# Performance work log

Measured on AMD Instinct MI355X. Metric: run time of the kernel, lower is better.

The kernel has to match this reference:

```python
import jax, jax.numpy as jnp
import numpy as np

N_FM = 100000; N_TP = 4096; N_SM = 100000
IN_FM = 64; IN_SM = 32; IN_TP = 32; IN_GF = 64; HID = 128
E_QOQ = 1000000; E_BP = 1000000; E_CP = 500000; E_CD = 500000; E_RB = 1000000


def setup_inputs():
    key = jax.random.key(0)
    ks = jax.random.split(key, 32)
    rn = lambda k, s, sc=0.05: jax.random.normal(k, s, jnp.float32) * sc
    inp = {}
    inp['x_fm'] = jax.random.normal(ks[0], (N_FM, IN_FM), jnp.float32)
    inp['x_sm'] = jax.random.normal(ks[1], (N_SM, IN_SM), jnp.float32)
    inp['period_vol'] = jax.random.uniform(ks[2], (N_TP, 1), jnp.float32)
    inp['gf'] = jax.random.normal(ks[3], (1, IN_GF), jnp.float32)
    inp['pe_table'] = rn(ks[4], (N_TP, IN_TP), 1.0)  # period_emb weight
    inp['qoq_src'] = jax.random.randint(ks[5], (E_QOQ,), 0, N_FM)
    inp['qoq_dst'] = jax.random.randint(ks[6], (E_QOQ,), 0, N_FM)
    inp['bp_src'] = jax.random.randint(ks[7], (E_BP,), 0, N_FM)
    inp['bp_dst'] = jax.random.randint(ks[8], (E_BP,), 0, N_TP)
    inp['cp_src'] = jax.random.randint(ks[9], (E_CP,), 0, N_TP)
    inp['cp_dst'] = jax.random.randint(ks[10], (E_CP,), 0, N_FM)
    inp['cd_src'] = jax.random.randint(ks[11], (E_CD,), 0, N_TP)
    inp['cd_dst'] = jax.random.randint(ks[12], (E_CD,), 0, N_SM)
    inp['rb_src'] = jax.random.randint(ks[13], (E_RB,), 0, N_TP)
    inp['rb_dst'] = jax.random.randint(ks[14], (E_RB,), 0, N_FM)
    i = 15
    # per-relation SAGEConv params: W_l [in_src,H] + bias, W_r [in_dst,H] (root, no bias)
    for name, ins, ind in [('qoq', IN_FM, IN_FM), ('bp', IN_FM, IN_TP), ('cp', IN_TP, IN_FM), ('cd', IN_TP, IN_SM), ('rb', IN_TP, IN_FM)]:
        inp[name + '_Wl'] = rn(ks[i], (ins, HID)); inp[name + '_bl'] = jnp.zeros((HID,), jnp.float32)
        inp[name + '_Wr'] = rn(ks[i + 1], (ind, HID)); i += 2
    for t in ['fm', 'tp', 'sm']:
        inp['ln_' + t + '_g'] = jnp.ones((HID,), jnp.float32)
        inp['ln_' + t + '_b'] = jnp.zeros((HID,), jnp.float32)
    inp['head_W1'] = rn(ks[i], (HID * 3 + IN_GF, HID // 2)); inp['head_b1'] = jnp.zeros((HID // 2,), jnp.float32)
    inp['head_W2'] = rn(ks[i + 1], (HID // 2, 1)); inp['head_b2'] = jnp.zeros((1,), jnp.float32)
    return inp


def _seg_mean(feat, dst, n):
    s = jax.ops.segment_sum(feat, dst, num_segments=n)
    c = jax.ops.segment_sum(jnp.ones((dst.shape[0], 1), feat.dtype), dst, num_segments=n)
    return s / jnp.maximum(c, 1.0)


def _sage(x_src, x_dst, src, dst, Wl, bl, Wr):
    # PyG SAGEConv: lin_l(mean_j x_j) + lin_r(x_i); aggregate raw features, then transform
    m = _seg_mean(x_src[src], dst, x_dst.shape[0])
    return m @ Wl + bl + x_dst @ Wr


def _ln(x, g, b, eps=1e-5):
    mu = x.mean(-1, keepdims=True)
    xc = x - mu
    var = (xc * xc).mean(-1, keepdims=True)
    return xc / jnp.sqrt(var + eps) * g + b


def _forward(x_fm, x_sm, period_vol, gf, pe_table,
             qoq_Wl, qoq_bl, qoq_Wr, bp_Wl, bp_bl, bp_Wr, cp_Wl, cp_bl, cp_Wr,
             cd_Wl, cd_bl, cd_Wr, rb_Wl, rb_bl, rb_Wr,
             ln_fm_g, ln_fm_b, ln_tp_g, ln_tp_b, ln_sm_g, ln_sm_b,
             head_W1, head_b1, head_W2, head_b2,
             qoq_src, qoq_dst, bp_src, bp_dst, cp_src, cp_dst, cd_src, cd_dst, rb_src, rb_dst):
    pe = pe_table * period_vol  # [T, in_tp]
    # HeteroConv aggr='mean': average relation outputs per destination type
    out_fm = (_sage(x_fm, x_fm, qoq_src, qoq_dst, qoq_Wl, qoq_bl, qoq_Wr)
              + _sage(pe, x_fm, cp_src, cp_dst, cp_Wl, cp_bl, cp_Wr)
              + _sage(pe, x_fm, rb_src, rb_dst, rb_Wl, rb_bl, rb_Wr)) / 3.0
    out_tp = _sage(x_fm, pe, bp_src, bp_dst, bp_Wl, bp_bl, bp_Wr)
    out_sm = _sage(pe, x_sm, cd_src, cd_dst, cd_Wl, cd_bl, cd_Wr)
    fm = jax.nn.relu(_ln(out_fm, ln_fm_g, ln_fm_b))
    tp = jax.nn.relu(_ln(out_tp, ln_tp_g, ln_tp_b))
    sm = jax.nn.relu(_ln(out_sm, ln_sm_g, ln_sm_b))
    h = jnp.concatenate([fm.mean(0), tp.mean(0), sm.mean(0), gf[0]], axis=-1)
    h = jax.nn.relu(h @ head_W1 + head_b1)  # dropout is identity in eval
    return (h @ head_W2 + head_b2).squeeze()


def reference(x_fm, x_sm, period_vol, gf, pe_table,
              qoq_src, qoq_dst, bp_src, bp_dst, cp_src, cp_dst, cd_src, cd_dst, rb_src, rb_dst,
              qoq_Wl, qoq_bl, qoq_Wr, bp_Wl, bp_bl, bp_Wr, cp_Wl, cp_bl, cp_Wr,
              cd_Wl, cd_bl, cd_Wr, rb_Wl, rb_bl, rb_Wr,
              ln_fm_g, ln_fm_b, ln_tp_g, ln_tp_b, ln_sm_g, ln_sm_b,
              head_W1, head_b1, head_W2, head_b2):
    return _forward(x_fm, x_sm, period_vol, gf, pe_table,
                    qoq_Wl, qoq_bl, qoq_Wr, bp_Wl, bp_bl, bp_Wr, cp_Wl, cp_bl, cp_Wr,
                    cd_Wl, cd_bl, cd_Wr, rb_Wl, rb_bl, rb_Wr,
                    ln_fm_g, ln_fm_b, ln_tp_g, ln_tp_b, ln_sm_g, ln_sm_b,
                    head_W1, head_b1, head_W2, head_b2,
                    qoq_src, qoq_dst, bp_src, bp_dst, cp_src, cp_dst, cd_src, cd_dst, rb_src, rb_dst)
```

## Files before the change

kernel.cpp:

```cpp
#include <hip/hip_runtime.h>
#include <hip/hip_fp16.h>

#define N_FM 100000
#define N_TP 4096
#define N_SM 100000
#define HID 128
#define E_QOQ 1000000
#define E_BP 1000000
#define E_CP 500000
#define E_CD 500000
#define E_RB 1000000
#define E_TOT 4000000

#define EO_CP  1000000
#define EO_RB  1500000
#define EO_BP  2500000
#define EO_CD  3500000

#define EL_QOQ 0
#define EL_CP  (N_FM)
#define EL_RB  (2 * N_FM)
#define EL_BP  (3 * N_FM)
#define EL_CD  (3 * N_FM + N_TP)
#define NTOT   (3 * N_FM + N_TP + N_SM)

#define BB_QOQ 0
#define BB_CP  782
#define BB_RB  1173
#define BB_BP  1564
#define BB_CD  1692
#define NBUCK  2083
#define CHUNK  4096
#define NCHUNK ((E_TOT + CHUNK - 1) / CHUNK)
#define EPB    (CHUNK / 256)

#define PAIRS_CAP 5784064

#define GRID_FM 768
#define GRID_TP 64
#define GRID_SM 1024

__device__ __forceinline__ int bucket_base(int b) {
    if (b < BB_CP) return b * 2048;
    if (b < BB_RB) return 1601536 + (b - BB_CP) * 2048;
    if (b < BB_BP) return 2402304 + (b - BB_RB) * 3584;
    if (b < BB_CD) return 3803648 + (b - BB_BP) * 9216;
    return 4983296 + (b - BB_CD) * 2048;
}

typedef _Float16 h2 __attribute__((ext_vector_type(2)));
typedef _Float16 f16x8_t __attribute__((ext_vector_type(8)));
typedef float f32x4_t __attribute__((ext_vector_type(4)));

union U32H2 { unsigned u; h2 h; };
union U4H8 { uint4 u; f16x8_t h; };

#if defined(__has_builtin)
#if __has_builtin(__builtin_amdgcn_fdot2)
#define HAVE_FDOT2 1
#endif
#endif

__device__ __forceinline__ unsigned pk2(float a, float b) {
    U32H2 x; x.h = h2{(_Float16)a, (_Float16)b}; return x.u;
}
__device__ __forceinline__ f16x8_t as_h8(uint4 v) { U4H8 x; x.u = v; return x.h; }

__device__ __forceinline__ float dot2sel(float acc, h2 v, h2 sel) {
#ifdef HAVE_FDOT2
    return __builtin_amdgcn_fdot2(v, sel, acc, false);
#else
    return acc + (float)v[0] * (float)sel[0] + (float)v[1] * (float)sel[1];
#endif
}

#define R1 (N_FM * 16)
#define R2 (R1 + N_SM * 8)
#define R3 (R2 + N_TP * 8)
#define R4 (R3 + 12288)
#define R5 (R4 + 6144)
#define R6 (R5 + 4096)
#define R7 (R6 + 128)

__device__ __forceinline__ unsigned pack_pair(const float* W, int p, int c) {
    return pk2(W[(2 * p) * HID + c], W[(2 * p + 1) * HID + c]);
}

__global__ void pack_all(const float* __restrict__ x_fm, const float* __restrict__ x_sm,
                         const float* __restrict__ pe_table, const float* __restrict__ pvol,
                         const float* __restrict__ qoq_Wl, const float* __restrict__ cp_Wl,
                         const float* __restrict__ rb_Wl, const float* __restrict__ qoq_Wr,
                         const float* __restrict__ cp_Wr, const float* __restrict__ rb_Wr,
                         const float* __restrict__ bp_Wl, const float* __restrict__ bp_Wr,
                         const float* __restrict__ cd_Wl, const float* __restrict__ cd_Wr,
                         const float* __restrict__ qoq_bl, const float* __restrict__ cp_bl,
                         const float* __restrict__ rb_bl,
                         unsigned* __restrict__ x_fm_f, unsigned* __restrict__ x_sm_f,
                         unsigned* __restrict__ pe_f, unsigned* __restrict__ wf_fm,
                         unsigned* __restrict__ wf_tp, unsigned* __restrict__ wf_sm,
                         float* __restrict__ bias_fm) {
    int gid = blockIdx.x * blockDim.x + threadIdx.x;
    if (gid < R1) {
        float4 t = ((const float4*)x_fm)[gid];
        uint2 o; o.x = pk2(t.x, t.y); o.y = pk2(t.z, t.w);
        ((uint2*)x_fm_f)[gid] = o;
    } else if (gid < R2) {
        int i = gid - R1;
        float4 t = ((const float4*)x_sm)[i];
        uint2 o; o.x = pk2(t.x, t.y); o.y = pk2(t.z, t.w);
        ((uint2*)x_sm_f)[i] = o;
    } else if (gid < R3) {
        int i = gid - R2;
        float4 t = ((const float4*)pe_table)[i];
        float v = pvol[i >> 3];
        uint2 o; o.x = pk2(t.x * v, t.y * v); o.y = pk2(t.z * v, t.w * v);
        ((uint2*)pe_f)[i] = o;
    } else if (gid < R4) {
        int j = gid - R3;
        int f = j >> 8, lr = (j >> 2) & 63, jj = j & 3;
        int p = (f >> 3) * 16 + ((lr >> 4) << 2) + jj;
        int c = (f & 7) * 16 + (lr & 15);
        unsigned v;
        if (p < 32) v = pack_pair(qoq_Wl, p, c);
        else if (p < 48) v = pack_pair(cp_Wl, p - 32, c);
        else if (p < 64) v = pack_pair(rb_Wl, p - 48, c);
        else {
            int pp = p - 64;
            float u0 = qoq_Wr[(2 * pp) * HID + c] + cp_Wr[(2 * pp) * HID + c] + rb_Wr[(2 * pp) * HID + c];
            float u1 = qoq_Wr[(2 * pp + 1) * HID + c] + cp_Wr[(2 * pp + 1) * HID + c] + rb_Wr[(2 * pp + 1) * HID + c];
            v = pk2(u0, u1);
        }
        wf_fm[j] = v;
    } else if (gid < R5) {
        int j = gid - R4;
        int f = j >> 8, lr = (j >> 2) & 63, jj = j & 3;
        int p = (f >> 3) * 16 + ((lr >> 4) << 2) + jj;
        int c = (f & 7) * 16 + (lr & 15);
        wf_tp[j] = (p < 32) ? pack_pair(bp_Wl, p, c) : pack_pair(bp_Wr, p - 32, c);
    } else if (gid < R6) {
        int j = gid - R5;
        int f = j >> 8, lr = (j >> 2) & 63, jj = j & 3;
        int p = (f >> 3) * 16 + ((lr >> 4) << 2) + jj;
        int c = (f & 7) * 16 + (lr & 15);
        wf_sm[j] = (p < 16) ? pack_pair(cd_Wl, p, c) : pack_pair(cd_Wr, p - 16, c);
    } else if (gid < R7) {
        int c = gid - R6;
        bias_fm[c] = qoq_bl[c] + cp_bl[c] + rb_bl[c];
    }
}

struct EdgePtrs {
    const int *qs, *qd, *cs, *cd_, *rs, *rd, *bs, *bd, *ds, *dd;
};

template <bool NEED_SRC>
__device__ __forceinline__ void edge_decode(const EdgePtrs& P, int e, int& bucket, int& dl, int& src) {
    const int* dp = P.qd; const int* sp = P.qs;
    int i = e, bb = BB_QOQ, sh = 7;
    if (e >= EO_CP) { i = e - EO_CP; dp = P.cd_; sp = P.cs; bb = BB_CP; sh = 8; }
    if (e >= EO_RB) { i = e - EO_RB; dp = P.rd;  sp = P.rs; bb = BB_RB; sh = 8; }
    if (e >= EO_BP) { i = e - EO_BP; dp = P.bd;  sp = P.bs; bb = BB_BP; sh = 5; }
    if (e >= EO_CD) { i = e - EO_CD; dp = P.dd;  sp = P.ds; bb = BB_CD; sh = 8; }
    int d = dp[i];
    bucket = bb + (d >> sh);
    dl = d & ((1 << sh) - 1);
    if (NEED_SRC) src = sp[i];
}

__global__ void __launch_bounds__(256) bin_kernel(EdgePtrs P, int* __restrict__ bwork,
                                                  unsigned* __restrict__ pairs) {
    __shared__ int lh[NBUCK];
    const int tid = threadIdx.x;
    for (int i = tid; i < NBUCK; i += 256) lh[i] = 0;
    __syncthreads();
    const int base = blockIdx.x * CHUNK;
    const int lim = min(base + CHUNK, E_TOT);
    unsigned ebd[EPB]; int esr[EPB];
#pragma unroll
    for (int j = 0; j < EPB; j++) {
        int e = base + tid + j * 256;
        if (e < lim) {
            int b, dl, s;
            edge_decode<true>(P, e, b, dl, s);
            ebd[j] = ((unsigned)b << 8) | (unsigned)dl;
            esr[j] = s;
            atomicAdd(&lh[b], 1);
        }
    }
    __syncthreads();
#pragma unroll
    for (int u = 0; u < (NBUCK + 255) / 256; u++) {
        int b = tid + u * 256;
        if (b < NBUCK) {
            int c = lh[b];
            lh[b] = c ? bucket_base(b) + atomicAdd(&bwork[b], c) : 0;
        }
    }
    __syncthreads();
#pragma unroll
    for (int j = 0; j < EPB; j++) {
        int e = base + tid + j * 256;
        if (e < lim) {
            int b = (int)(ebd[j] >> 8);
            int pos = atomicAdd(&lh[b], 1);
            pairs[pos] = ((ebd[j] & 255u) << 24) | (unsigned)esr[j];
        }
    }
}

__global__ void __launch_bounds__(256) esort(const int* __restrict__ bwork,
                                             const unsigned* __restrict__ pairs,
                                             int* __restrict__ so,
                                             int* __restrict__ el_beg, int* __restrict__ el_end) {
    __shared__ int hist[256];
    __shared__ int wsum[4];
    __shared__ int so_lds[9216];
    const int b = blockIdx.x;
    const int tid = threadIdx.x;
    const int lane = tid & 63, wv = tid >> 6;
    int beg = bucket_base(b);
    int end = beg + bwork[b];
    int egbase, ne;
    if (b < BB_CP)      { int e0 = (b - BB_QOQ) << 7; egbase = EL_QOQ + e0; ne = min(128, N_FM - e0); }
    else if (b < BB_RB) { int e0 = (b - BB_CP) << 8;  egbase = EL_CP + e0;  ne = min(256, N_FM - e0); }
    else if (b < BB_BP) { int e0 = (b - BB_RB) << 8;  egbase = EL_RB + e0;  ne = min(256, N_FM - e0); }
    else if (b < BB_CD) { int e0 = (b - BB_BP) << 5;  egbase = EL_BP + e0;  ne = min(32, N_TP - e0); }
    else                { int e0 = (b - BB_CD) << 8;  egbase = EL_CD + e0;  ne = min(256, N_SM - e0); }
    hist[tid] = 0;
    __syncthreads();
    for (int e = beg + tid; e < end; e += 256)
        atomicAdd(&hist[pairs[e] >> 24], 1);
    __syncthreads();
    int v = hist[tid];
    int x = v;
#pragma unroll
    for (int off = 1; off < 64; off <<= 1) {
        int u = __shfl_up(x, off);
        if (lane >= off) x += u;
    }
    if (lane == 63) wsum[wv] = x;
    __syncthreads();
    int wbase = 0;
#pragma unroll
    for (int w = 0; w < 4; w++) wbase += (w < wv) ? wsum[w] : 0;
    int excl = wbase + x - v;
    if (tid < ne) {
        el_beg[egbase + tid] = beg + excl;
        el_end[egbase + tid] = beg + excl + v;
    }
    hist[tid] = excl;
    __syncthreads();
    for (int e = beg + tid; e < end; e += 256) {
        unsigned pr = pairs[e];
        int dl = pr >> 24;
        int pos = atomicAdd(&hist[dl], 1);
        so_lds[pos] = (int)(pr & 0xFFFFFF);
    }
    __syncthreads();
    const int n = end - beg;
    for (int i = tid; i < n; i += 256) so[beg + i] = so_lds[i];
}

template <int LOGP, int NPRO>
__device__ __forceinline__ void gather_one(int g, int lane, const int* __restrict__ begs,
                                           const int* __restrict__ ends,
                                           const int* __restrict__ ssrc,
                                           const unsigned* __restrict__ feat,
                                           unsigned* __restrict__ mean) {
    const int P = 1 << LOGP;
    const h2 SLO = h2{(_Float16)1.0f, (_Float16)0.0f};
    const h2 SHI = h2{(_Float16)0.0f, (_Float16)1.0f};
    int beg = begs[g], end = ends[g];
    int n = end - beg;
    float alo = 0.0f, ahi = 0.0f;
    if (n > 0) {
        const int nm1 = n - 1;
        int s[NPRO];
#pragma unroll
        for (int j = 0; j < NPRO; j++) s[j] = ssrc[beg + min(j, nm1)];
        unsigned v[NPRO];
#pragma unroll
        for (int j = 0; j < NPRO; j++) v[j] = feat[(size_t)(unsigned)s[j] * P + lane];
#pragma unroll
        for (int j = 0; j < NPRO; j++) {
            U32H2 u; u.u = (j < n) ? v[j] : 0u;
            alo = dot2sel(alo, u.h, SLO); ahi = dot2sel(ahi, u.h, SHI);
        }
        int i = beg + NPRO;
        for (; i + 8 <= end; i += 8) {
            int t0 = ssrc[i],     t1 = ssrc[i + 1], t2 = ssrc[i + 2], t3 = ssrc[i + 3];
            int t4 = ssrc[i + 4], t5 = ssrc[i + 5], t6 = ssrc[i + 6], t7 = ssrc[i + 7];
            unsigned w0 = feat[(size_t)t0 * P + lane];
            unsigned w1 = feat[(size_t)t1 * P + lane];
            unsigned w2 = feat[(size_t)t2 * P + lane];
            unsigned w3 = feat[(size_t)t3 * P + lane];
            unsigned w4 = feat[(size_t)t4 * P + lane];
            unsigned w5 = feat[(size_t)t5 * P + lane];
            unsigned w6 = feat[(size_t)t6 * P + lane];
            unsigned w7 = feat[(size_t)t7 * P + lane];
            U32H2 u;
            u.u = w0; alo = dot2sel(alo, u.h, SLO); ahi = dot2sel(ahi, u.h, SHI);
            u.u = w1; alo = dot2sel(alo, u.h, SLO); ahi = dot2sel(ahi, u.h, SHI);
            u.u = w2; alo = dot2sel(alo, u.h, SLO); ahi = dot2sel(ahi, u.h, SHI);
            u.u = w3; alo = dot2sel(alo, u.h, SLO); ahi = dot2sel(ahi, u.h, SHI);
            u.u = w4; alo = dot2sel(alo, u.h, SLO); ahi = dot2sel(ahi, u.h, SHI);
            u.u = w5; alo = dot2sel(alo, u.h, SLO); ahi = dot2sel(ahi, u.h, SHI);
            u.u = w6; alo = dot2sel(alo, u.h, SLO); ahi = dot2sel(ahi, u.h, SHI);
            u.u = w7; alo = dot2sel(alo, u.h, SLO); ahi = dot2sel(ahi, u.h, SHI);
        }
        for (; i < end; i++) {
            U32H2 u; u.u = feat[(size_t)ssrc[i] * P + lane];
            alo = dot2sel(alo, u.h, SLO); ahi = dot2sel(ahi, u.h, SHI);
        }
    }
    float ic = (n > 0) ? 1.0f / (float)n : 0.0f;
    mean[(size_t)g * P + lane] = pk2(alo * ic, ahi * ic);
}

#define G1 (N_TP * 32)
#define G2 (G1 + N_FM * 32)
#define G3 (G2 + N_FM * 16)
#define G4 (G3 + N_SM * 16)
#define G5 (G4 + N_FM * 16)

__global__ void __launch_bounds__(256)
gather_all(const int* __restrict__ el_beg, const int* __restrict__ el_end,
           const int* __restrict__ so_all,
           const unsigned* __restrict__ x_fm_f, const unsigned* __restrict__ pe_f,
           unsigned* __restrict__ mean_qoq, unsigned* __restrict__ mean_cp,
           unsigned* __restrict__ mean_rb, unsigned* __restrict__ mean_bp,
           unsigned* __restrict__ mean_cd) {
    int gid = blockIdx.x * blockDim.x + threadIdx.x;
    if (gid < G1) {
        gather_one<5, 16>(gid >> 5, gid & 31, el_beg + EL_BP, el_end + EL_BP, so_all, x_fm_f, mean_bp);
    } else if (gid < G2) {
        int i = gid - G1;
        gather_one<5, 16>(i >> 5, i & 31, el_beg + EL_QOQ, el_end + EL_QOQ, so_all, x_fm_f, mean_qoq);
    } else if (gid < G3) {
        int i = gid - G2;
        gather_one<4, 8>(i >> 4, i & 15, el_beg + EL_CP, el_end + EL_CP, so_all, pe_f, mean_cp);
    } else if (gid < G4) {
        int i = gid - G3;
        gather_one<4, 8>(i >> 4, i & 15, el_beg + EL_CD, el_end + EL_CD, so_all, pe_f, mean_cd);
    } else if (gid < G5) {
        int i = gid - G4;
        gather_one<4, 16>(i >> 4, i & 15, el_beg + EL_RB, el_end + EL_RB, so_all, pe_f, mean_rb);
    }
}


__global__ void __launch_bounds__(256)
fm_mfma(const unsigned* __restrict__ mq, const unsigned* __restrict__ mc,
        const unsigned* __restrict__ mr, const unsigned* __restrict__ xf,
        const unsigned* __restrict__ wfrag, const float* __restrict__ bias,
        const float* __restrict__ ln_g, const float* __restrict__ ln_b,
        float* __restrict__ part) {
    __shared__ uint4 wlds[48 * 64];
    const int tid = threadIdx.x, lane = tid & 63, wid = tid >> 6;
    for (int i = tid; i < 48 * 64; i += 256) wlds[i] = ((const uint4*)wfrag)[i];
    const int c0 = lane & 15, ko = lane >> 4;
    float bias_[8], g_[8], b_[8], colacc[8];
#pragma unroll
    for (int nt = 0; nt < 8; nt++) {
        int c = nt * 16 + c0;
        bias_[nt] = bias[c]; g_[nt] = ln_g[c]; b_[nt] = ln_b[c]; colacc[nt] = 0.0f;
    }
    __syncthreads();
    const f32x4_t zero = {0.0f, 0.0f, 0.0f, 0.0f};
    const int ntiles = N_FM / 16;
    for (int tile = blockIdx.x * 4 + wid; tile < ntiles; tile += gridDim.x * 4) {
        const size_t row = (size_t)tile * 16 + c0;
        uint4 av[6];
        av[0] = ((const uint4*)mq)[row * 8 + ko];
        av[1] = ((const uint4*)mq)[row * 8 + 4 + ko];
        av[2] = ((const uint4*)mc)[row * 4 + ko];
        av[3] = ((const uint4*)mr)[row * 4 + ko];
        av[4] = ((const uint4*)xf)[row * 8 + ko];
        av[5] = ((const uint4*)xf)[row * 8 + 4 + ko];
        f32x4_t acc[8];
#pragma unroll
        for (int nt = 0; nt < 8; nt++) acc[nt] = zero;
#pragma unroll
        for (int ks = 0; ks < 6; ks++) {
            f16x8_t af = as_h8(av[ks]);
#pragma unroll
            for (int nt = 0; nt < 8; nt++)
                acc[nt] = __builtin_amdgcn_mfma_f32_16x16x32_f16(
                    af, as_h8(wlds[(ks * 8 + nt) * 64 + lane]), acc[nt], 0, 0, 0);
        }
#pragma unroll
        for (int r = 0; r < 4; r++) {
            float yv[8]; float s = 0.0f, q = 0.0f;
#pragma unroll
            for (int nt = 0; nt < 8; nt++) {
                float y = (acc[nt][r] + bias_[nt]) * (1.0f / 3.0f);
                yv[nt] = y; s += y; q += y * y;
            }
#pragma unroll
            for (int off = 1; off < 16; off <<= 1) { s += __shfl_xor(s, off); q += __shfl_xor(q, off); }
            float mu = s * (1.0f / 128.0f);
            float var = fmaxf(q * (1.0f / 128.0f) - mu * mu, 0.0f);
            float rs = rsqrtf(var + 1e-5f);
#pragma unroll
            for (int nt = 0; nt < 8; nt++)
                colacc[nt] += fmaxf((yv[nt] - mu) * rs * g_[nt] + b_[nt], 0.0f);
        }
    }
#pragma unroll
    for (int nt = 0; nt < 8; nt++) {
        colacc[nt] += __shfl_xor(colacc[nt], 16);
        colacc[nt] += __shfl_xor(colacc[nt], 32);
    }
    __syncthreads();
    float* sred = (float*)wlds;
    if (lane < 16) {
#pragma unroll
        for (int nt = 0; nt < 8; nt++) sred[wid * 128 + nt * 16 + lane] = colacc[nt];
    }
    __syncthreads();
    if (tid < 128)
        part[(size_t)blockIdx.x * 128 + tid] =
            sred[tid] + sred[128 + tid] + sred[256 + tid] + sred[384 + tid];
}

template <int KSA, int KSB>
__global__ void __launch_bounds__(256)
rows_mfma(int ntiles, const unsigned* __restrict__ mA, const unsigned* __restrict__ xB,
          const unsigned* __restrict__ wfrag, const float* __restrict__ bl,
          const float* __restrict__ ln_g, const float* __restrict__ ln_b,
          float* __restrict__ part) {
    constexpr int KS = KSA + KSB;
    __shared__ uint4 wlds[KS * 8 * 64];
    const int tid = threadIdx.x, lane = tid & 63, wid = tid >> 6;
    for (int i = tid; i < KS * 8 * 64; i += 256) wlds[i] = ((const uint4*)wfrag)[i];
    const int c0 = lane & 15, ko = lane >> 4;
    float bias_[8], g_[8], b_[8], colacc[8];
#pragma unroll
    for (int nt = 0; nt < 8; nt++) {
        int c = nt * 16 + c0;
        bias_[nt] = bl[c]; g_[nt] = ln_g[c]; b_[nt] = ln_b[c]; colacc[nt] = 0.0f;
    }
    __syncthreads();
    const f32x4_t zero = {0.0f, 0.0f, 0.0f, 0.0f};
    for (int tile = blockIdx.x * 4 + wid; tile < ntiles; tile += gridDim.x * 4) {
        const size_t row = (size_t)tile * 16 + c0;
        uint4 av[KS];
#pragma unroll
        for (int ks = 0; ks < KSA; ks++) av[ks] = ((const uint4*)mA)[row * (KSA * 4) + ks * 4 + ko];
#pragma unroll
        for (int ks = 0; ks < KSB; ks++) av[KSA + ks] = ((const uint4*)xB)[row * (KSB * 4) + ks * 4 + ko];
        f32x4_t acc[8];
#pragma unroll
        for (int nt = 0; nt < 8; nt++) acc[nt] = zero;
#pragma unroll
        for (int ks = 0; ks < KS; ks++) {
            f16x8_t af = as_h8(av[ks]);
#pragma unroll
            for (int nt = 0; nt < 8; nt++)
                acc[nt] = __builtin_amdgcn_mfma_f32_16x16x32_f16(
                    af, as_h8(wlds[(ks * 8 + nt) * 64 + lane]), acc[nt], 0, 0, 0);
        }
#pragma unroll
        for (int r = 0; r < 4; r++) {
            float yv[8]; float s = 0.0f, q = 0.0f;
#pragma unroll
            for (int nt = 0; nt < 8; nt++) {
                float y = acc[nt][r] + bias_[nt];
                yv[nt] = y; s += y; q += y * y;
            }
#pragma unroll
            for (int off = 1; off < 16; off <<= 1) { s += __shfl_xor(s, off); q += __shfl_xor(q, off); }
            float mu = s * (1.0f / 128.0f);
            float var = fmaxf(q * (1.0f / 128.0f) - mu * mu, 0.0f);
            float rs = rsqrtf(var + 1e-5f);
#pragma unroll
            for (int nt = 0; nt < 8; nt++)
                colacc[nt] += fmaxf((yv[nt] - mu) * rs * g_[nt] + b_[nt], 0.0f);
        }
    }
#pragma unroll
    for (int nt = 0; nt < 8; nt++) {
        colacc[nt] += __shfl_xor(colacc[nt], 16);
        colacc[nt] += __shfl_xor(colacc[nt], 32);
    }
    __syncthreads();
    float* sred = (float*)wlds;
    if (lane < 16) {
#pragma unroll
        for (int nt = 0; nt < 8; nt++) sred[wid * 128 + nt * 16 + lane] = colacc[nt];
    }
    __syncthreads();
    if (tid < 128)
        part[(size_t)blockIdx.x * 128 + tid] =
            sred[tid] + sred[128 + tid] + sred[256 + tid] + sred[384 + tid];
}

__global__ void __launch_bounds__(512)
reduce_cols(const float* __restrict__ part, float* __restrict__ colsum) {
    __shared__ float lds[512];
    const int t = threadIdx.x, col = t & 127, sl = t >> 7;
    int cnt, srcoff, dst;
    if (blockIdx.x == 0)      { cnt = GRID_FM; srcoff = 0;                         dst = 0;   }
    else if (blockIdx.x == 1) { cnt = GRID_TP; srcoff = GRID_FM * 128;             dst = 128; }
    else                      { cnt = GRID_SM; srcoff = (GRID_FM + GRID_TP) * 128; dst = 256; }
    float a = 0.0f;
    for (int i = sl; i < cnt; i += 4) a += part[srcoff + i * 128 + col];
    lds[t] = a;
    __syncthreads();
    if (t < 128) colsum[dst + t] = lds[t] + lds[128 + t] + lds[256 + t] + lds[384 + t];
}

__global__ void head_kernel(const float* __restrict__ colsum, const float* __restrict__ gf,
                            const float* __restrict__ W1, const float* __restrict__ b1,
                            const float* __restrict__ W2, const float* __restrict__ b2,
                            float* __restrict__ out) {
    __shared__ float h[448];
    __shared__ float sh[512];
    __shared__ float h1[64];
    int t = threadIdx.x;
    if (t < 128) h[t] = colsum[t] * (1.0f / N_FM);
    else if (t < 256) h[t] = colsum[t] * (1.0f / N_TP);
    else if (t < 384) h[t] = colsum[t] * (1.0f / N_SM);
    else if (t < 448) h[t] = gf[t - 384];
    __syncthreads();
    {
        int col = t & 63, slice = t >> 6;
        float a = 0.0f;
        for (int k = slice * 56; k < slice * 56 + 56; k++) a += h[k] * W1[k * 64 + col];
        sh[slice * 64 + col] = a;
    }
    __syncthreads();
    if (t < 64) {
        float a = b1[t];
#pragma unroll
        for (int s = 0; s < 8; s++) a += sh[s * 64 + t];
        h1[t] = fmaxf(a, 0.0f);
    }
    __syncthreads();
    if (t < 64) {
        float p = h1[t] * W2[t];
#pragma unroll
        for (int off = 1; off < 64; off <<= 1) p += __shfl_xor(p, off);
        if (t == 0) out[0] = p + b2[0];
    }
}

extern "C" void kernel_launch(void* const* d_in, const int* in_sizes, int n_in,
                              void* d_out, int out_size, void* d_ws, size_t ws_size,
                              hipStream_t stream) {
    const float* x_fm = (const float*)d_in[0];
    const float* x_sm = (const float*)d_in[1];
    const float* period_vol = (const float*)d_in[2];
    const float* gf = (const float*)d_in[3];
    const float* pe_table = (const float*)d_in[4];
    const int* qoq_src = (const int*)d_in[5];
    const int* qoq_dst = (const int*)d_in[6];
    const int* bp_src = (const int*)d_in[7];
    const int* bp_dst = (const int*)d_in[8];
    const int* cp_src = (const int*)d_in[9];
    const int* cp_dst = (const int*)d_in[10];
    const int* cd_src = (const int*)d_in[11];
    const int* cd_dst = (const int*)d_in[12];
    const int* rb_src = (const int*)d_in[13];
    const int* rb_dst = (const int*)d_in[14];
    const float* qoq_Wl = (const float*)d_in[15];
    const float* qoq_bl = (const float*)d_in[16];
    const float* qoq_Wr = (const float*)d_in[17];
    const float* bp_Wl = (const float*)d_in[18];
    const float* bp_bl = (const float*)d_in[19];
    const float* bp_Wr = (const float*)d_in[20];
    const float* cp_Wl = (const float*)d_in[21];
    const float* cp_bl = (const float*)d_in[22];
    const float* cp_Wr = (const float*)d_in[23];
    const float* cd_Wl = (const float*)d_in[24];
    const float* cd_bl = (const float*)d_in[25];
    const float* cd_Wr = (const float*)d_in[26];
    const float* rb_Wl = (const float*)d_in[27];
    const float* rb_bl = (const float*)d_in[28];
    const float* rb_Wr = (const float*)d_in[29];
    const float* ln_fm_g = (const float*)d_in[30];
    const float* ln_fm_b = (const float*)d_in[31];
    const float* ln_tp_g = (const float*)d_in[32];
    const float* ln_tp_b = (const float*)d_in[33];
    const float* ln_sm_g = (const float*)d_in[34];
    const float* ln_sm_b = (const float*)d_in[35];
    const float* head_W1 = (const float*)d_in[36];
    const float* head_b1 = (const float*)d_in[37];
    const float* head_W2 = (const float*)d_in[38];
    const float* head_b2 = (const float*)d_in[39];

    unsigned* wsu = (unsigned*)d_ws;
    size_t off = 0;
    int* bwork = (int*)(wsu + off); off += NBUCK;
    float* colsum = (float*)(wsu + off); off += 384;
    size_t zero_words = off;
    off = (off + 3) & ~(size_t)3;
    unsigned* pairs = wsu + off; off += PAIRS_CAP;
    int* so_all = (int*)(wsu + off); off += PAIRS_CAP;
    int* el_beg = (int*)(wsu + off); off += NTOT;
    int* el_end = (int*)(wsu + off); off += NTOT;
    unsigned* mean_qoq = wsu + off; off += (size_t)N_FM * 32;
    unsigned* mean_cp  = wsu + off; off += (size_t)N_FM * 16;
    unsigned* mean_rb  = wsu + off; off += (size_t)N_FM * 16;
    unsigned* mean_bp  = wsu + off; off += (size_t)N_TP * 32;
    unsigned* mean_cd  = wsu + off; off += (size_t)N_SM * 16;
    unsigned* pe_f     = wsu + off; off += (size_t)N_TP * 16;
    unsigned* x_fm_f   = wsu + off; off += (size_t)N_FM * 32;
    unsigned* x_sm_f   = wsu + off; off += (size_t)N_SM * 16;
    unsigned* wf_fm    = wsu + off; off += 12288;
    unsigned* wf_tp    = wsu + off; off += 6144;
    unsigned* wf_sm    = wsu + off; off += 4096;
    float* bias_fm     = (float*)(wsu + off); off += 128;

    float* part_fm = (float*)pairs;
    float* part_tp = part_fm + GRID_FM * 128;
    float* part_sm = part_tp + GRID_TP * 128;

    hipMemsetAsync(d_ws, 0, zero_words * 4, stream);

    pack_all<<<(R7 + 255) / 256, 256, 0, stream>>>(
        x_fm, x_sm, pe_table, period_vol, qoq_Wl, cp_Wl, rb_Wl, qoq_Wr, cp_Wr, rb_Wr,
        bp_Wl, bp_Wr, cd_Wl, cd_Wr, qoq_bl, cp_bl, rb_bl,
        x_fm_f, x_sm_f, pe_f, wf_fm, wf_tp, wf_sm, bias_fm);

    EdgePtrs EP{qoq_src, qoq_dst, cp_src, cp_dst, rb_src, rb_dst, bp_src, bp_dst, cd_src, cd_dst};

    bin_kernel<<<NCHUNK, 256, 0, stream>>>(EP, bwork, pairs);
    esort<<<NBUCK, 256, 0, stream>>>(bwork, pairs, so_all, el_beg, el_end);
    gather_all<<<(G5 + 255) / 256, 256, 0, stream>>>(el_beg, el_end, so_all, x_fm_f, pe_f,
                                                     mean_qoq, mean_cp, mean_rb, mean_bp, mean_cd);

    fm_mfma<<<GRID_FM, 256, 0, stream>>>(mean_qoq, mean_cp, mean_rb, x_fm_f, wf_fm,
                                         bias_fm, ln_fm_g, ln_fm_b, part_fm);
    rows_mfma<2, 1><<<GRID_TP, 256, 0, stream>>>(N_TP / 16, mean_bp, pe_f, wf_tp,
                                                 bp_bl, ln_tp_g, ln_tp_b, part_tp);
    rows_mfma<1, 1><<<GRID_SM, 256, 0, stream>>>(N_SM / 16, mean_cd, x_sm_f, wf_sm,
                                                 cd_bl, ln_sm_g, ln_sm_b, part_sm);

    reduce_cols<<<3, 512, 0, stream>>>(part_fm, colsum);

    head_kernel<<<1, 512, 0, stream>>>(colsum, gf, head_W1, head_b1, head_W2, head_b2,
                                       (float*)d_out);
}
```

Measured before the change: 428.2 us.

## Fuse bucket sort and neighbor gather into one kernel using LDS-resident indices

Merges the per-bucket counting sort with the mean-aggregation gather, so each block sorts its bucket's edges into LDS and immediately gathers source features for its destination nodes. This removes the global writes and reads of the sorted source array and the per-node begin/end offsets, and drops one kernel launch. In exchange the gather parallelism is now tied to one block per bucket, and the large LDS allocation (about 38 KB) limits occupancy, which may reduce latency hiding for the random feature loads.

New measurement: 446.1 us. 4.2% more time.

```diff
diff --git a/kernel.cpp b/kernel.cpp
--- a/kernel.cpp
+++ b/kernel.cpp
@@ -208,24 +208,72 @@
     }
 }
 
-__global__ void __launch_bounds__(256) esort(const int* __restrict__ bwork,
-                                             const unsigned* __restrict__ pairs,
-                                             int* __restrict__ so,
-                                             int* __restrict__ el_beg, int* __restrict__ el_end) {
+template <int LOGP, int NPRO>
+__device__ __forceinline__ void bucket_gather(int ne, size_t gbase, const int* __restrict__ ebeg,
+                                              const int* __restrict__ ecnt,
+                                              const int* __restrict__ so_lds,
+                                              const unsigned* __restrict__ feat,
+                                              unsigned* __restrict__ mean, int tid) {
+    const int P = 1 << LOGP;
+    const int NG = 256 >> LOGP;
+    const int grp = tid >> LOGP, fl = tid & (P - 1);
+    const h2 SLO = h2{(_Float16)1.0f, (_Float16)0.0f};
+    const h2 SHI = h2{(_Float16)0.0f, (_Float16)1.0f};
+    for (int dl = grp; dl < ne; dl += NG) {
+        int bgl = ebeg[dl], n = ecnt[dl];
+        float alo = 0.0f, ahi = 0.0f;
+        if (n > 0) {
+            const int nm1 = n - 1;
+            int s[NPRO];
+#pragma unroll
+            for (int j = 0; j < NPRO; j++) s[j] = so_lds[bgl + min(j, nm1)];
+            unsigned v[NPRO];
+#pragma unroll
+            for (int j = 0; j < NPRO; j++) v[j] = feat[(size_t)(unsigned)s[j] * P + fl];
+#pragma unroll
+            for (int j = 0; j < NPRO; j++) {
+                U32H2 u; u.u = (j < n) ? v[j] : 0u;
+                alo = dot2sel(alo, u.h, SLO); ahi = dot2sel(ahi, u.h, SHI);
+            }
+            for (int i = NPRO; i < n; i += 8) {
+                int t_[8]; unsigned w_[8];
+#pragma unroll
+                for (int j = 0; j < 8; j++) t_[j] = so_lds[bgl + min(i + j, nm1)];
+#pragma unroll
+                for (int j = 0; j < 8; j++) w_[j] = feat[(size_t)(unsigned)t_[j] * P + fl];
+#pragma unroll
+                for (int j = 0; j < 8; j++) {
+                    U32H2 u; u.u = (i + j < n) ? w_[j] : 0u;
+                    alo = dot2sel(alo, u.h, SLO); ahi = dot2sel(ahi, u.h, SHI);
+                }
+            }
+        }
+        float ic = (n > 0) ? 1.0f / (float)n : 0.0f;
+        mean[(gbase + (size_t)dl) * P + fl] = pk2(alo * ic, ahi * ic);
+    }
+}
+
+__global__ void __launch_bounds__(256)
+esga(const int* __restrict__ bwork, const unsigned* __restrict__ pairs,
+     const unsigned* __restrict__ x_fm_f, const unsigned* __restrict__ pe_f,
+     unsigned* __restrict__ mean_qoq, unsigned* __restrict__ mean_cp,
+     unsigned* __restrict__ mean_rb, unsigned* __restrict__ mean_bp,
+     unsigned* __restrict__ mean_cd) {
     __shared__ int hist[256];
     __shared__ int wsum[4];
+    __shared__ int ebeg[256];
+    __shared__ int ecnt[256];
     __shared__ int so_lds[9216];
-    const int b = blockIdx.x;
-    const int tid = threadIdx.x;
+    const int b = blockIdx.x, tid = threadIdx.x;
     const int lane = tid & 63, wv = tid >> 6;
     int beg = bucket_base(b);
     int end = beg + bwork[b];
-    int egbase, ne;
-    if (b < BB_CP)      { int e0 = (b - BB_QOQ) << 7; egbase = EL_QOQ + e0; ne = min(128, N_FM - e0); }
-    else if (b < BB_RB) { int e0 = (b - BB_CP) << 8;  egbase = EL_CP + e0;  ne = min(256, N_FM - e0); }
-    else if (b < BB_BP) { int e0 = (b - BB_RB) << 8;  egbase = EL_RB + e0;  ne = min(256, N_FM - e0); }
-    else if (b < BB_CD) { int e0 = (b - BB_BP) << 5;  egbase = EL_BP + e0;  ne = min(32, N_TP - e0); }
-    else                { int e0 = (b - BB_CD) << 8;  egbase = EL_CD + e0;  ne = min(256, N_SM - e0); }
+    int e0, ne, cls;
+    if (b < BB_CP)      { e0 = (b - BB_QOQ) << 7; ne = min(128, N_FM - e0); cls = 0; }
+    else if (b < BB_RB) { e0 = (b - BB_CP) << 8;  ne = min(256, N_FM - e0); cls = 1; }
+    else if (b < BB_BP) { e0 = (b - BB_RB) << 8;  ne = min(256, N_FM - e0); cls = 2; }
+    else if (b < BB_CD) { e0 = (b - BB_BP) << 5;  ne = min(32, N_TP - e0);  cls = 3; }
+    else                { e0 = (b - BB_CD) << 8;  ne = min(256, N_SM - e0); cls = 4; }
     hist[tid] = 0;
     __syncthreads();
     for (int e = beg + tid; e < end; e += 256)
@@ -244,10 +292,8 @@
 #pragma unroll
     for (int w = 0; w < 4; w++) wbase += (w < wv) ? wsum[w] : 0;
     int excl = wbase + x - v;
-    if (tid < ne) {
-        el_beg[egbase + tid] = beg + excl;
-        el_end[egbase + tid] = beg + excl + v;
-    }
+    ebeg[tid] = excl;
+    ecnt[tid] = v;
     hist[tid] = excl;
     __syncthreads();
     for (int e = beg + tid; e < end; e += 256) {
@@ -257,95 +303,11 @@
         so_lds[pos] = (int)(pr & 0xFFFFFF);
     }
     __syncthreads();
-    const int n = end - beg;
-    for (int i = tid; i < n; i += 256) so[beg + i] = so_lds[i];
-}
-
-template <int LOGP, int NPRO>
-__device__ __forceinline__ void gather_one(int g, int lane, const int* __restrict__ begs,
-                                           const int* __restrict__ ends,
-                                           const int* __restrict__ ssrc,
-                                           const unsigned* __restrict__ feat,
-                                           unsigned* __restrict__ mean) {
-    const int P = 1 << LOGP;
-    const h2 SLO = h2{(_Float16)1.0f, (_Float16)0.0f};
-    const h2 SHI = h2{(_Float16)0.0f, (_Float16)1.0f};
-    int beg = begs[g], end = ends[g];
-    int n = end - beg;
-    float alo = 0.0f, ahi = 0.0f;
-    if (n > 0) {
-        const int nm1 = n - 1;
-        int s[NPRO];
-#pragma unroll
-        for (int j = 0; j < NPRO; j++) s[j] = ssrc[beg + min(j, nm1)];
-        unsigned v[NPRO];
-#pragma unroll
-        for (int j = 0; j < NPRO; j++) v[j] = feat[(size_t)(unsigned)s[j] * P + lane];
-#pragma unroll
-        for (int j = 0; j < NPRO; j++) {
-            U32H2 u; u.u = (j < n) ? v[j] : 0u;
-            alo = dot2sel(alo, u.h, SLO); ahi = dot2sel(ahi, u.h, SHI);
-        }
-        int i = beg + NPRO;
-        for (; i + 8 <= end; i += 8) {
-            int t0 = ssrc[i],     t1 = ssrc[i + 1], t2 = ssrc[i + 2], t3 = ssrc[i + 3];
-            int t4 = ssrc[i + 4], t5 = ssrc[i + 5], t6 = ssrc[i + 6], t7 = ssrc[i + 7];
-            unsigned w0 = feat[(size_t)t0 * P + lane];
-            unsigned w1 = feat[(size_t)t1 * P + lane];
-            unsigned w2 = feat[(size_t)t2 * P + lane];
-            unsigned w3 = feat[(size_t)t3 * P + lane];
-            unsigned w4 = feat[(size_t)t4 * P + lane];
-            unsigned w5 = feat[(size_t)t5 * P + lane];
-            unsigned w6 = feat[(size_t)t6 * P + lane];
-            unsigned w7 = feat[(size_t)t7 * P + lane];
-            U32H2 u;
-            u.u = w0; alo = dot2sel(alo, u.h, SLO); ahi = dot2sel(ahi, u.h, SHI);
-            u.u = w1; alo = dot2sel(alo, u.h, SLO); ahi = dot2sel(ahi, u.h, SHI);
-            u.u = w2; alo = dot2sel(alo, u.h, SLO); ahi = dot2sel(ahi, u.h, SHI);
-            u.u = w3; alo = dot2sel(alo, u.h, SLO); ahi = dot2sel(ahi, u.h, SHI);
-            u.u = w4; alo = dot2sel(alo, u.h, SLO); ahi = dot2sel(ahi, u.h, SHI);
-            u.u = w5; alo = dot2sel(alo, u.h, SLO); ahi = dot2sel(ahi, u.h, SHI);
-            u.u = w6; alo = dot2sel(alo, u.h, SLO); ahi = dot2sel(ahi, u.h, SHI);
-            u.u = w7; alo = dot2sel(alo, u.h, SLO); ahi = dot2sel(ahi, u.h, SHI);
-        }
-        for (; i < end; i++) {
-            U32H2 u; u.u = feat[(size_t)ssrc[i] * P + lane];
-            alo = dot2sel(alo, u.h, SLO); ahi = dot2sel(ahi, u.h, SHI);
-        }
-    }
-    float ic = (n > 0) ? 1.0f / (float)n : 0.0f;
-    mean[(size_t)g * P + lane] = pk2(alo * ic, ahi * ic);
-}
-
-#define G1 (N_TP * 32)
-#define G2 (G1 + N_FM * 32)
-#define G3 (G2 + N_FM * 16)
-#define G4 (G3 + N_SM * 16)
-#define G5 (G4 + N_FM * 16)
-
-__global__ void __launch_bounds__(256)
-gather_all(const int* __restrict__ el_beg, const int* __restrict__ el_end,
-           const int* __restrict__ so_all,
-           const unsigned* __restrict__ x_fm_f, const unsigned* __restrict__ pe_f,
-           unsigned* __restrict__ mean_qoq, unsigned* __restrict__ mean_cp,
-           unsigned* __restrict__ mean_rb, unsigned* __restrict__ mean_bp,
-           unsigned* __restrict__ mean_cd) {
-    int gid = blockIdx.x * blockDim.x + threadIdx.x;
-    if (gid < G1) {
-        gather_one<5, 16>(gid >> 5, gid & 31, el_beg + EL_BP, el_end + EL_BP, so_all, x_fm_f, mean_bp);
-    } else if (gid < G2) {
-        int i = gid - G1;
-        gather_one<5, 16>(i >> 5, i & 31, el_beg + EL_QOQ, el_end + EL_QOQ, so_all, x_fm_f, mean_qoq);
-    } else if (gid < G3) {
-        int i = gid - G2;
-        gather_one<4, 8>(i >> 4, i & 15, el_beg + EL_CP, el_end + EL_CP, so_all, pe_f, mean_cp);
-    } else if (gid < G4) {
-        int i = gid - G3;
-        gather_one<4, 8>(i >> 4, i & 15, el_beg + EL_CD, el_end + EL_CD, so_all, pe_f, mean_cd);
-    } else if (gid < G5) {
-        int i = gid - G4;
-        gather_one<4, 16>(i >> 4, i & 15, el_beg + EL_RB, el_end + EL_RB, so_all, pe_f, mean_rb);
-    }
+    if (cls == 0)      bucket_gather<5, 16>(ne, (size_t)e0, ebeg, ecnt, so_lds, x_fm_f, mean_qoq, tid);
+    else if (cls == 1) bucket_gather<4, 8>(ne, (size_t)e0, ebeg, ecnt, so_lds, pe_f, mean_cp, tid);
+    else if (cls == 2) bucket_gather<4, 16>(ne, (size_t)e0, ebeg, ecnt, so_lds, pe_f, mean_rb, tid);
+    else if (cls == 3) bucket_gather<5, 16>(ne, (size_t)e0, ebeg, ecnt, so_lds, x_fm_f, mean_bp, tid);
+    else               bucket_gather<4, 8>(ne, (size_t)e0, ebeg, ecnt, so_lds, pe_f, mean_cd, tid);
 }
 
 
@@ -596,9 +558,6 @@
     size_t zero_words = off;
     off = (off + 3) & ~(size_t)3;
     unsigned* pairs = wsu + off; off += PAIRS_CAP;
-    int* so_all = (int*)(wsu + off); off += PAIRS_CAP;
-    int* el_beg = (int*)(wsu + off); off += NTOT;
-    int* el_end = (int*)(wsu + off); off += NTOT;
     unsigned* mean_qoq = wsu + off; off += (size_t)N_FM * 32;
     unsigned* mean_cp  = wsu + off; off += (size_t)N_FM * 16;
     unsigned* mean_rb  = wsu + off; off += (size_t)N_FM * 16;
@@ -626,9 +585,8 @@
     EdgePtrs EP{qoq_src, qoq_dst, cp_src, cp_dst, rb_src, rb_dst, bp_src, bp_dst, cd_src, cd_dst};
 
     bin_kernel<<<NCHUNK, 256, 0, stream>>>(EP, bwork, pairs);
-    esort<<<NBUCK, 256, 0, stream>>>(bwork, pairs, so_all, el_beg, el_end);
-    gather_all<<<(G5 + 255) / 256, 256, 0, stream>>>(el_beg, el_end, so_all, x_fm_f, pe_f,
-                                                     mean_qoq, mean_cp, mean_rb, mean_bp, mean_cd);
+    esga<<<NBUCK, 256, 0, stream>>>(bwork, pairs, x_fm_f, pe_f,
+                                    mean_qoq, mean_cp, mean_rb, mean_bp, mean_cd);
 
     fm_mfma<<<GRID_FM, 256, 0, stream>>>(mean_qoq, mean_cp, mean_rb, x_fm_f, wf_fm,
                                          bias_fm, ln_fm_g, ln_fm_b, part_fm);
```
